# Performance work log

Hardware: AMD Instinct MI355X
Metric: run time of the kernel (lower is better)

Reference implementation:

```python
import jax, jax.numpy as jnp
import numpy as np

B, T, V, E, H = 64, 512, 32000, 256, 512


def setup_inputs() -> dict:
    key = jax.random.key(0)
    k0, k1, k2, k3 = jax.random.split(key, 4)
    sequence_input = jax.random.randint(k0, (B, T), 0, V)
    emb_table = jax.random.normal(k1, (V, E), dtype=jnp.float32) * 0.02
    Wx = jax.random.normal(k2, (E, 4 * H), dtype=jnp.float32) * (1.0 / np.sqrt(E))
    Wh = jax.random.normal(k3, (H, 4 * H), dtype=jnp.float32) * (1.0 / np.sqrt(H))
    # Keras unit_forget_bias=True: forget-gate bias initialized to 1
    b = jnp.zeros((4 * H,), dtype=jnp.float32).at[H:2 * H].set(1.0)
    return {"sequence_input": sequence_input, "emb_table": emb_table,
            "Wx": Wx, "Wh": Wh, "b": b}


def _lstm(xz, Wh):
    # xz: [T, B, 4H] precomputed input projections (+bias); scan the recurrence.
    h0 = jnp.zeros((xz.shape[1], H), dtype=xz.dtype)
    c0 = jnp.zeros_like(h0)

    def step(carry, z_t):
        h, c = carry
        z = z_t + h @ Wh                      # [B, 4H]
        i, f, g, o = jnp.split(z, 4, axis=-1)  # Keras gate order: i, f, c(g), o
        i = jax.nn.sigmoid(i)
        f = jax.nn.sigmoid(f)
        g = jnp.tanh(g)
        o = jax.nn.sigmoid(o)
        c = f * c + i * g
        h = o * jnp.tanh(c)
        return (h, c), h

    (h_last, _c), seq = jax.lax.scan(step, (h0, c0), xz)
    return seq, h_last


def reference(sequence_input, emb_table, Wx, Wh, b):
    x = emb_table[sequence_input]                     # [B, T, E]
    xz = jnp.einsum('bte,eg->btg', x, Wx) + b         # [B, T, 4H]
    seq, h_last = _lstm(jnp.swapaxes(xz, 0, 1), Wh)   # seq: [T, B, H]
    seq = jnp.swapaxes(seq, 0, 1)                     # [B, T, H]
    mask = (sequence_input != 0).astype(jnp.float32)[..., None]  # [B, T, 1]
    return seq, h_last, mask
```

## Files before the change

kernel.cpp:

```cpp
#include <hip/hip_runtime.h>
#include <stdint.h>

#define B_   64
#define T_   512
#define E_   256
#define H_   512
#define G4_  2048
#define V_   32000

#define OUT_SEQ   0
#define OUT_HLAST 16777216
#define OUT_MASK  16809984

#define OFF_EMB  0u
#define OFF_WXT  16384000u
#define OFF_WHT  17432576u
#define OFF_C    19529728u
#define OFF_XZ   19660800u
#define XZ_PER_T   262144u
#define RING_PER_T  65536u
#define SLOT_U64    8192


#define POISON64 0xFFFFFFFFFFFFFFFFULL

typedef short bf16x8 __attribute__((ext_vector_type(8)));
typedef float f32x4  __attribute__((ext_vector_type(4)));
typedef unsigned int u32x4 __attribute__((ext_vector_type(4)));

__device__ __forceinline__ unsigned short f2bf(float f) {
  uint32_t u = __float_as_uint(f);
  u = (u + 0x7FFFu + ((u >> 16) & 1u)) >> 16;
  return (unsigned short)u;
}
__device__ __forceinline__ float bf2f(unsigned short h) {
  return __uint_as_float(((uint32_t)h) << 16);
}
__device__ __forceinline__ float sigmoid_f(float x) {
  return __fdividef(1.f, 1.f + __expf(-x));
}
__device__ __forceinline__ float tanh_f(float x) {
  return 1.f - __fdividef(2.f, 1.f + __expf(2.f * x));
}

__global__ void k_prep_emb(const float* __restrict__ emb, unsigned short* __restrict__ out) {
  int i = (blockIdx.x * 256 + threadIdx.x) * 4;
  if (i < V_ * E_) {
    float4 v = *(const float4*)(emb + i);
    ushort4 o;
    o.x = f2bf(v.x); o.y = f2bf(v.y); o.z = f2bf(v.z); o.w = f2bf(v.w);
    *(ushort4*)(out + i) = o;
  }
}

__global__ void k_prep_w(const float* __restrict__ Wx, const float* __restrict__ Wh,
                         unsigned short* __restrict__ wxt, unsigned short* __restrict__ wht) {
  int i = blockIdx.x * 256 + threadIdx.x;
  if (i < 524288) {
    int n = i >> 8, k = i & 255;
    wxt[i] = f2bf(Wx[k * G4_ + n]);
  } else if (i < 524288 + 1048576) {
    int j = i - 524288;
    int n = j >> 9, k = j & 511;
    wht[j] = f2bf(Wh[k * G4_ + n]);
  }
}

__global__ void k_mask(const int* __restrict__ seq, float* __restrict__ out) {
  int i = blockIdx.x * 256 + threadIdx.x;
  if (i < B_ * T_) out[OUT_MASK + i] = (seq[i] != 0) ? 1.f : 0.f;
}

__global__ __launch_bounds__(256) void k_copyseq(const unsigned int* __restrict__ ring,
                                                 float* __restrict__ out, int t0, int R) {
  int t = t0 + blockIdx.x;
  const unsigned int* src = ring + (size_t)(t % R) * (SLOT_U64 * 2);
  for (int i = threadIdx.x; i < B_ * H_ / 2; i += 256) {
    int b = i >> 8;
    int j = (i & 255) * 2;
    unsigned int v = src[((((b >> 4) * 64 + (j >> 3)) * 16 + (b & 15)) * 4) + ((j >> 1) & 3)];
    float2 o;
    o.x = bf2f((unsigned short)(v & 0xFFFFu));
    o.y = bf2f((unsigned short)(v >> 16));
    *(float2*)(out + ((size_t)b * T_ + t) * H_ + j) = o;
  }
}

__global__ void k_hlast(const unsigned int* __restrict__ ring, float* __restrict__ out, int R) {
  int i = blockIdx.x * 256 + threadIdx.x;
  if (i < B_ * H_) {
    int b = i >> 9, j = i & 511;
    unsigned int v = ring[(size_t)((T_ - 1) % R) * (SLOT_U64 * 2) +
                          ((((b >> 4) * 64 + (j >> 3)) * 16 + (b & 15)) * 4) + ((j >> 1) & 3)];
    out[OUT_HLAST + i] = bf2f((unsigned short)((j & 1) ? (v >> 16) : (v & 0xFFFFu)));
  }
}

#define LDA_ 264
__global__ __launch_bounds__(256) void k_gemm_xz(
    const int* __restrict__ seq, const unsigned short* __restrict__ embb,
    const unsigned short* __restrict__ wxt, const float* __restrict__ bias,
    unsigned short* __restrict__ xz, int t0) {
  __shared__ __align__(16) unsigned short a_lds[128 * LDA_];
  __shared__ __align__(16) unsigned short b_lds[128 * LDA_];
  int bx = blockIdx.x & 15;
  int by = blockIdx.x >> 4;
  int tid = threadIdx.x;

  {
    int r = tid >> 1, half = tid & 1;
    int m = by * 128 + r;
    int t = t0 + (m >> 6), b = m & 63;
    int idx = seq[b * T_ + t];
    const unsigned short* srcA = embb + (size_t)idx * E_ + half * 128;
    const unsigned short* srcB = wxt + (size_t)(bx * 128 + r) * E_ + half * 128;
    unsigned short* dstA = a_lds + r * LDA_ + half * 128;
    unsigned short* dstB = b_lds + r * LDA_ + half * 128;
#pragma unroll
    for (int q = 0; q < 16; ++q) {
      *(bf16x8*)(dstA + q * 8) = *(const bf16x8*)(srcA + q * 8);
      *(bf16x8*)(dstB + q * 8) = *(const bf16x8*)(srcB + q * 8);
    }
  }
  __syncthreads();

  int w = tid >> 6, lane = tid & 63;
  int l15 = lane & 15, l4 = lane >> 4;
  int wm = w >> 1, wn = w & 1;
  f32x4 acc[4][4] = {};
#pragma unroll
  for (int ks = 0; ks < 8; ++ks) {
    bf16x8 a[4], bb[4];
#pragma unroll
    for (int mf = 0; mf < 4; ++mf)
      a[mf] = *(const bf16x8*)(a_lds + (wm * 64 + mf * 16 + l15) * LDA_ + ks * 32 + 8 * l4);
#pragma unroll
    for (int nf = 0; nf < 4; ++nf)
      bb[nf] = *(const bf16x8*)(b_lds + (wn * 64 + nf * 16 + l15) * LDA_ + ks * 32 + 8 * l4);
#pragma unroll
    for (int mf = 0; mf < 4; ++mf)
#pragma unroll
      for (int nf = 0; nf < 4; ++nf)
        acc[mf][nf] = __builtin_amdgcn_mfma_f32_16x16x32_bf16(a[mf], bb[nf], acc[mf][nf], 0, 0, 0);
  }
#pragma unroll
  for (int nf = 0; nf < 4; ++nf) {
    int n = bx * 128 + wn * 64 + nf * 16 + l15;
    float bv = bias[n];
#pragma unroll
    for (int mf = 0; mf < 4; ++mf)
#pragma unroll
      for (int q = 0; q < 4; ++q) {
        int m = by * 128 + wm * 64 + mf * 16 + l4 * 4 + q;
        xz[(size_t)m * G4_ + n] = f2bf(acc[mf][nf][q] + bv);
      }
  }
}

__global__ __launch_bounds__(128, 1) void k_lstm(
    const unsigned short* __restrict__ wht, const unsigned short* __restrict__ xz,
    unsigned long long* hring, float* cbuf, int t0, int tend, int R) {
  int bid = blockIdx.x;
  int g = bid & 3, nwg = bid >> 2;
  int J0 = nwg * 32;
  int tid = threadIdx.x;
  int w = tid >> 6, lane = tid & 63;
  int l15 = lane & 15, l4 = lane >> 4;
  int bglob0 = g * 16;
  int jcol = J0 + w * 16 + l15;

  u32x4 Bs[4][16];
#pragma unroll
  for (int gt = 0; gt < 4; ++gt)
#pragma unroll
    for (int ks = 0; ks < 16; ++ks) {
      Bs[gt][ks] = *(const u32x4*)(wht + (size_t)(gt * 512 + jcol) * H_ + ks * 32 + l4 * 8);
      asm volatile("" : "+v"(Bs[gt][ks]));
    }

  float c4[4];
  if (t0 == 0) {
    c4[0] = c4[1] = c4[2] = c4[3] = 0.f;
  } else {
#pragma unroll
    for (int q = 0; q < 4; ++q) c4[q] = cbuf[(bglob0 + l4 * 4 + q) * H_ + jcol];
  }

  size_t pbase = ((size_t)(g * 64 + (jcol >> 3)) * 16) * 2 + ((jcol >> 2) & 1);
  size_t rbyte = ((size_t)(g * 64 + l4) * 32 + l15 * 2) * 8;

  int xoff[16];
#pragma unroll
  for (int gt = 0; gt < 4; ++gt)
#pragma unroll
    for (int q = 0; q < 4; ++q)
      xoff[gt * 4 + q] = (l4 * 4 + q) * G4_ + gt * 512 + jcol;

  float xzf[16];
  {
    const unsigned short* x0 = xz + (size_t)bglob0 * G4_;
#pragma unroll
    for (int k = 0; k < 16; ++k) xzf[k] = bf2f(x0[xoff[k]]);
  }

  int t = t0;
  if (t0 == 0) {
    unsigned long long* hdst = hring;
#pragma unroll
    for (int q = 0; q < 4; ++q) {
      float ig = sigmoid_f(xzf[0 * 4 + q]);
      float gg = tanh_f(xzf[2 * 4 + q]);
      float og = sigmoid_f(xzf[3 * 4 + q]);
      float cn = ig * gg;
      c4[q] = cn;
      float hv = og * tanh_f(cn);
      unsigned int my = f2bf(hv);
      unsigned int p1 = __shfl_xor(my, 1);
      unsigned int pair = my | (p1 << 16);
      unsigned int hi2 = __shfl_xor(pair, 2);
      if ((l15 & 3) == 0) {
        unsigned long long vv = (unsigned long long)pair | ((unsigned long long)hi2 << 32);
        __hip_atomic_store(&hdst[pbase + (size_t)(l4 * 4 + q) * 2], vv,
                           __ATOMIC_RELAXED, __HIP_MEMORY_SCOPE_AGENT);
      }
    }
    t = 1;
    if (t < tend) {
      const unsigned short* x1 = xz + ((size_t)1 * B_ + bglob0) * G4_;
#pragma unroll
      for (int k = 0; k < 16; ++k) xzf[k] = bf2f(x1[xoff[k]]);
    }
  }

  for (; t < tend; ++t) {
    f32x4 accA[4], accB[4];
#pragma unroll
    for (int gt = 0; gt < 4; ++gt)
#pragma unroll
      for (int q = 0; q < 4; ++q) { accA[gt][q] = xzf[gt * 4 + q]; accB[gt][q] = 0.f; }

    const char* hb = (const char*)hring + ((size_t)((t - 1) % R) * SLOT_U64) * 8 + rbyte;
    u32x4 v4[16];
    while (true) {
#pragma unroll
      for (int ks = 0; ks < 16; ++ks)
        asm volatile("global_load_dwordx4 %0, %1, off sc0 sc1"
                     : "=v"(v4[ks]) : "v"(hb + (size_t)ks * 1024));
      asm volatile("s_waitcnt vmcnt(0)" ::: "memory");
      __builtin_amdgcn_sched_barrier(0);
      bool ok = true;
#pragma unroll
      for (int ks = 0; ks < 16; ++ks)
        ok &= (v4[ks][0] != 0xFFFFFFFFu) & (v4[ks][2] != 0xFFFFFFFFu);
      if (__all(ok)) break;
      __builtin_amdgcn_s_sleep(1);
    }
    __builtin_amdgcn_sched_barrier(0);
    asm volatile("" ::: "memory");

    unsigned int raw[16];
    const unsigned short* xn = xz + ((size_t)(t + 1 - t0) * B_ + bglob0) * G4_;
    if (t + 1 < tend) {
#pragma unroll
      for (int k = 0; k < 16; ++k) raw[k] = xn[xoff[k]];
    }
    __builtin_amdgcn_sched_barrier(0);

#pragma unroll
    for (int ks = 0; ks < 16; ++ks) {
      bf16x8 a = __builtin_bit_cast(bf16x8, v4[ks]);
      if (ks & 1) {
#pragma unroll
        for (int gt = 0; gt < 4; ++gt)
          accB[gt] = __builtin_amdgcn_mfma_f32_16x16x32_bf16(
              a, __builtin_bit_cast(bf16x8, Bs[gt][ks]), accB[gt], 0, 0, 0);
      } else {
#pragma unroll
        for (int gt = 0; gt < 4; ++gt)
          accA[gt] = __builtin_amdgcn_mfma_f32_16x16x32_bf16(
              a, __builtin_bit_cast(bf16x8, Bs[gt][ks]), accA[gt], 0, 0, 0);
      }
    }

    unsigned long long* hdst = hring + (size_t)(t % R) * SLOT_U64;
#pragma unroll
    for (int q = 0; q < 4; ++q) {
      float zi = accA[0][q] + accB[0][q];
      float zf = accA[1][q] + accB[1][q];
      float zg = accA[2][q] + accB[2][q];
      float zo = accA[3][q] + accB[3][q];
      float ig = sigmoid_f(zi);
      float fg = sigmoid_f(zf);
      float gg = tanh_f(zg);
      float og = sigmoid_f(zo);
      float cn = fg * c4[q] + ig * gg;
      c4[q] = cn;
      float hv = og * tanh_f(cn);
      unsigned int my = f2bf(hv);
      unsigned int p1 = __shfl_xor(my, 1);
      unsigned int pair = my | (p1 << 16);
      unsigned int hi2 = __shfl_xor(pair, 2);
      if ((l15 & 3) == 0) {
        unsigned long long vv = (unsigned long long)pair | ((unsigned long long)hi2 << 32);
        __hip_atomic_store(&hdst[pbase + (size_t)(l4 * 4 + q) * 2], vv,
                           __ATOMIC_RELAXED, __HIP_MEMORY_SCOPE_AGENT);
      }
    }

    if (t + 1 < tend) {
#pragma unroll
      for (int k = 0; k < 16; ++k) xzf[k] = __uint_as_float(raw[k] << 16);
    }
  }

#pragma unroll
  for (int q = 0; q < 4; ++q) cbuf[(bglob0 + l4 * 4 + q) * H_ + jcol] = c4[q];
}

extern "C" void kernel_launch(void* const* d_in, const int* in_sizes, int n_in,
                              void* d_out, int out_size, void* d_ws, size_t ws_size,
                              hipStream_t stream) {
  const int* seq    = (const int*)d_in[0];
  const float* emb  = (const float*)d_in[1];
  const float* Wx   = (const float*)d_in[2];
  const float* Wh   = (const float*)d_in[3];
  const float* bias = (const float*)d_in[4];
  float* out = (float*)d_out;
  char* ws = (char*)d_ws;

  unsigned short* embb = (unsigned short*)(ws + OFF_EMB);
  unsigned short* wxt  = (unsigned short*)(ws + OFF_WXT);
  unsigned short* wht  = (unsigned short*)(ws + OFF_WHT);
  float* cbuf          = (float*)(ws + OFF_C);
  unsigned short* xz   = (unsigned short*)(ws + OFF_XZ);

  size_t cap = (ws_size > OFF_XZ) ? (ws_size - OFF_XZ) : 0;
  int TC = (cap > RING_PER_T) ? (int)((cap - RING_PER_T) / (XZ_PER_T + RING_PER_T)) : 2;
  if (TC > T_) TC = T_;
  TC &= ~1;
  if (TC < 2) TC = 2;
  int R = TC + 1;
  unsigned long long* hring = (unsigned long long*)(ws + OFF_XZ + (size_t)TC * XZ_PER_T);

  k_prep_emb<<<dim3(8000), dim3(256), 0, stream>>>(emb, embb);
  k_prep_w<<<dim3(6144), dim3(256), 0, stream>>>(Wx, Wh, wxt, wht);
  k_mask<<<dim3(128), dim3(256), 0, stream>>>(seq, out);

  for (int t0 = 0; t0 < T_; t0 += TC) {
    int tc = T_ - t0; if (tc > TC) tc = TC;
    int s0 = t0 % R;
    if (s0 + tc <= R) {
      hipMemsetAsync((char*)hring + (size_t)s0 * RING_PER_T, 0xFF, (size_t)tc * RING_PER_T, stream);
    } else {
      hipMemsetAsync((char*)hring + (size_t)s0 * RING_PER_T, 0xFF, (size_t)(R - s0) * RING_PER_T, stream);
      hipMemsetAsync((char*)hring, 0xFF, (size_t)(s0 + tc - R) * RING_PER_T, stream);
    }
    k_gemm_xz<<<dim3((tc / 2) * 16), dim3(256), 0, stream>>>(seq, embb, wxt, bias, xz, t0);
    k_lstm<<<dim3(64), dim3(128), 0, stream>>>(wht, xz, (unsigned long long*)hring, cbuf, t0, t0 + tc, R);
    k_copyseq<<<dim3(tc), dim3(256), 0, stream>>>((const unsigned int*)hring, out, t0, R);
  }
  k_hlast<<<dim3(128), dim3(256), 0, stream>>>((const unsigned int*)hring, out, R);
}
```

Before: 1.689 ms.

## Split h-ring polling between two waves and exchange halves through LDS

Each of the two waves in a block now polls and loads only half of the previous hidden-state slice from the global ring (8 instead of 16 dwordx4 loads), then shares it with the other wave through a double-buffered LDS array after a workgroup barrier. The recurrent weight registers are permuted so each wave's own half is consumed first. The next-step xz prefetch is moved ahead of the spin loop so its latency overlaps the wait. This halves global/L2 polling traffic on the serial critical path but adds an LDS round trip and a block barrier every timestep.

```diff
diff --git a/kernel.cpp b/kernel.cpp
--- a/kernel.cpp
+++ b/kernel.cpp
@@ -160,6 +160,7 @@
 __global__ __launch_bounds__(128, 1) void k_lstm(
     const unsigned short* __restrict__ wht, const unsigned short* __restrict__ xz,
     unsigned long long* hring, float* cbuf, int t0, int tend, int R) {
+  __shared__ __align__(16) u32x4 hsh[2][16][64];
   int bid = blockIdx.x;
   int g = bid & 3, nwg = bid >> 2;
   int J0 = nwg * 32;
@@ -173,9 +174,10 @@
 #pragma unroll
   for (int gt = 0; gt < 4; ++gt)
 #pragma unroll
-    for (int ks = 0; ks < 16; ++ks) {
-      Bs[gt][ks] = *(const u32x4*)(wht + (size_t)(gt * 512 + jcol) * H_ + ks * 32 + l4 * 8);
-      asm volatile("" : "+v"(Bs[gt][ks]));
+    for (int lk = 0; lk < 16; ++lk) {
+      int phys = (lk < 8) ? (w * 8 + lk) : ((w ^ 1) * 8 + (lk - 8));
+      Bs[gt][lk] = *(const u32x4*)(wht + (size_t)(gt * 512 + jcol) * H_ + phys * 32 + l4 * 8);
+      asm volatile("" : "+v"(Bs[gt][lk]));
     }
 
   float c4[4];
@@ -187,7 +189,7 @@
   }
 
   size_t pbase = ((size_t)(g * 64 + (jcol >> 3)) * 16) * 2 + ((jcol >> 2) & 1);
-  size_t rbyte = ((size_t)(g * 64 + l4) * 32 + l15 * 2) * 8;
+  size_t rbyte = ((size_t)(g * 64 + l4) * 32 + l15 * 2) * 8 + (size_t)w * 8 * 1024;
 
   int xoff[16];
 #pragma unroll
@@ -239,46 +241,60 @@
 #pragma unroll
       for (int q = 0; q < 4; ++q) { accA[gt][q] = xzf[gt * 4 + q]; accB[gt][q] = 0.f; }
 
+    unsigned int raw[16];
+    const unsigned short* xn = xz + ((size_t)(t + 1 - t0) * B_ + bglob0) * G4_;
+    if (t + 1 < tend) {
+#pragma unroll
+      for (int k = 0; k < 16; ++k) raw[k] = xn[xoff[k]];
+    }
+    __builtin_amdgcn_sched_barrier(0);
+
     const char* hb = (const char*)hring + ((size_t)((t - 1) % R) * SLOT_U64) * 8 + rbyte;
-    u32x4 v4[16];
+    u32x4 vmy[8];
     while (true) {
 #pragma unroll
-      for (int ks = 0; ks < 16; ++ks)
+      for (int i = 0; i < 8; ++i)
         asm volatile("global_load_dwordx4 %0, %1, off sc0 sc1"
-                     : "=v"(v4[ks]) : "v"(hb + (size_t)ks * 1024));
+                     : "=v"(vmy[i]) : "v"(hb + (size_t)i * 1024));
       asm volatile("s_waitcnt vmcnt(0)" ::: "memory");
       __builtin_amdgcn_sched_barrier(0);
       bool ok = true;
 #pragma unroll
-      for (int ks = 0; ks < 16; ++ks)
-        ok &= (v4[ks][0] != 0xFFFFFFFFu) & (v4[ks][2] != 0xFFFFFFFFu);
+      for (int i = 0; i < 8; ++i)
+        ok &= (vmy[i][0] != 0xFFFFFFFFu) & (vmy[i][2] != 0xFFFFFFFFu);
       if (__all(ok)) break;
       __builtin_amdgcn_s_sleep(1);
     }
     __builtin_amdgcn_sched_barrier(0);
     asm volatile("" ::: "memory");
 
-    unsigned int raw[16];
-    const unsigned short* xn = xz + ((size_t)(t + 1 - t0) * B_ + bglob0) * G4_;
-    if (t + 1 < tend) {
-#pragma unroll
-      for (int k = 0; k < 16; ++k) raw[k] = xn[xoff[k]];
-    }
-    __builtin_amdgcn_sched_barrier(0);
-
-#pragma unroll
-    for (int ks = 0; ks < 16; ++ks) {
-      bf16x8 a = __builtin_bit_cast(bf16x8, v4[ks]);
-      if (ks & 1) {
+    {
+      u32x4* dst = &hsh[t & 1][w * 8][0];
+#pragma unroll
+      for (int i = 0; i < 8; ++i) dst[i * 64 + lane] = vmy[i];
+    }
+    asm volatile("s_waitcnt lgkmcnt(0)" ::: "memory");
+    __builtin_amdgcn_s_barrier();
+    u32x4 vot[8];
+    {
+      const u32x4* src = &hsh[t & 1][(w ^ 1) * 8][0];
+#pragma unroll
+      for (int i = 0; i < 8; ++i) vot[i] = src[i * 64 + lane];
+    }
+
+#pragma unroll
+    for (int lk = 0; lk < 16; ++lk) {
+      bf16x8 a = __builtin_bit_cast(bf16x8, (lk < 8) ? vmy[lk] : vot[lk - 8]);
+      if (lk & 1) {
 #pragma unroll
         for (int gt = 0; gt < 4; ++gt)
           accB[gt] = __builtin_amdgcn_mfma_f32_16x16x32_bf16(
-              a, __builtin_bit_cast(bf16x8, Bs[gt][ks]), accB[gt], 0, 0, 0);
+              a, __builtin_bit_cast(bf16x8, Bs[gt][lk]), accB[gt], 0, 0, 0);
       } else {
 #pragma unroll
         for (int gt = 0; gt < 4; ++gt)
           accA[gt] = __builtin_amdgcn_mfma_f32_16x16x32_bf16(
-              a, __builtin_bit_cast(bf16x8, Bs[gt][ks]), accA[gt], 0, 0, 0);
+              a, __builtin_bit_cast(bf16x8, Bs[gt][lk]), accA[gt], 0, 0, 0);
       }
     }
 
```

New measurement: 1.640 ms. 2.9% less time.
